# Optimization experiments

Hardware: AMD Instinct MI355X
Metric: run time of the kernel (lower is better)

Reference implementation:

```python
import jax, jax.numpy as jnp
import numpy as np

B, M, N_CTR, K = 16, 2048, 512, 32
DIM, DEPTH, HEADS = 384, 6, 6
EMB = 48  # fourier embedding dim (48//6 = 8 freqs per axis, basis [3,24])


def make_basis():
    e = (2.0 ** np.arange(EMB // 6)).astype(np.float32) * np.pi  # [8]
    z = np.zeros(EMB // 6, np.float32)
    basis = np.stack([np.concatenate([e, z, z]),
                      np.concatenate([z, e, z]),
                      np.concatenate([z, z, e])])  # [3, 24]
    return jnp.asarray(basis)


def fourier_embed(x, basis):
    # x [..., 3] -> [..., 48]  (sin/cos of 24 frequency projections)
    p = jnp.einsum('...d,de->...e', x, basis)
    return jnp.concatenate([jnp.sin(p), jnp.cos(p)], axis=-1)


def fps_idx(pos, n):
    # farthest point sampling, deterministic start at index 0. pos [M,3] -> [n]
    d0 = jnp.sum((pos - pos[0]) ** 2, -1)
    def step(d, _):
        i = jnp.argmax(d)
        d = jnp.minimum(d, jnp.sum((pos - pos[i]) ** 2, -1))
        return d, i
    _, idxs = jax.lax.scan(step, d0, None, length=n - 1)
    return jnp.concatenate([jnp.zeros(1, jnp.int32), idxs.astype(jnp.int32)])


def layernorm(x, g, b, eps=1e-6):
    m = jnp.mean(x, -1, keepdims=True)
    v = jnp.var(x, -1, keepdims=True)
    return (x - m) * jax.lax.rsqrt(v + eps) * g + b


def _lin(key, fi, fo):
    kw, kb = jax.random.split(key)
    w = jax.random.normal(kw, (fi, fo), jnp.float32) / np.sqrt(fi)
    b = jax.random.normal(kb, (fo,), jnp.float32) * 0.01
    return w, b


def setup_inputs() -> dict:
    key = jax.random.key(0)
    ks = jax.random.split(key, 16)
    pc = jax.random.uniform(ks[0], (B, M, 3), jnp.float32)
    embed_w, embed_b = _lin(ks[1], 3 + EMB, DIM)
    lw1, lb1 = _lin(ks[2], 3 + EMB, 256)
    lw2, lb2 = _lin(ks[3], 256, 256)
    gw1, gb1 = _lin(ks[4], 256, 256)
    gw2, gb2 = _lin(ks[5], 256, DIM)
    def stack_lin(k, fi, fo):
        kk = jax.random.split(k, DEPTH)
        ws, bs = zip(*[_lin(kk[i], fi, fo) for i in range(DEPTH)])
        return jnp.stack(ws), jnp.stack(bs)
    qkv_w, qkv_b = stack_lin(ks[6], DIM, 3 * DIM)
    proj_w, proj_b = stack_lin(ks[7], DIM, DIM)
    fc1_w, fc1_b = stack_lin(ks[8], DIM, 4 * DIM)
    fc2_w, fc2_b = stack_lin(ks[9], 4 * DIM, DIM)
    return dict(
        pc=pc, embed_w=embed_w, embed_b=embed_b,
        lw1=lw1, lb1=lb1, lw2=lw2, lb2=lb2,
        gw1=gw1, gb1=gb1, gw2=gw2, gb2=gb2,
        ln1_g=jnp.ones((DEPTH, DIM)), ln1_b=jnp.zeros((DEPTH, DIM)),
        qkv_w=qkv_w, qkv_b=qkv_b, proj_w=proj_w, proj_b=proj_b,
        gamma1=jax.random.normal(ks[10], (DEPTH, DIM)) * 0.1,
        ln2_g=jnp.ones((DEPTH, DIM)), ln2_b=jnp.zeros((DEPTH, DIM)),
        fc1_w=fc1_w, fc1_b=fc1_b, fc2_w=fc2_w, fc2_b=fc2_b,
        gamma2=jax.random.normal(ks[11], (DEPTH, DIM)) * 0.1,
        lnf_g=jnp.ones((DIM,)), lnf_b=jnp.zeros((DIM,)),
    )


def reference(pc, embed_w, embed_b, lw1, lb1, lw2, lb2, gw1, gb1, gw2, gb2,
              ln1_g, ln1_b, qkv_w, qkv_b, proj_w, proj_b, gamma1,
              ln2_g, ln2_b, fc1_w, fc1_b, fc2_w, fc2_b, gamma2, lnf_g, lnf_b):
    basis = make_basis()
    # --- FPS centers (per batch) ---
    idx = jax.vmap(lambda p: fps_idx(p, N_CTR))(pc)                 # [B,N]
    centers = jnp.take_along_axis(pc, idx[:, :, None], axis=1)      # [B,N,3]
    # --- KNN graph: for each center, K nearest of the M points ---
    d2 = jnp.sum((centers[:, :, None, :] - pc[:, None, :, :]) ** 2, -1)  # [B,N,M]
    _, nn_idx = jax.lax.top_k(-d2, K)                               # [B,N,K]
    # --- PointConv: gather -> local MLP -> max-scatter -> global MLP ---
    src = jax.vmap(lambda p, i: p[i])(pc, nn_idx)                   # [B,N,K,3]
    rel = src - centers[:, :, None, :]
    feat = jnp.concatenate([rel, fourier_embed(rel, basis)], -1)    # [B,N,K,51]
    h = jax.nn.relu(feat @ lw1 + lb1) @ lw2 + lb2                   # [B,N,K,256]
    h = jnp.max(h, axis=2)  # scatter_max over edges == max over K neighbors
    x = jax.nn.relu(h @ gw1 + gb1) @ gw2 + gb2                      # [B,N,DIM]
    # --- positional embedding tokens ---
    pe = jnp.concatenate([centers, fourier_embed(centers, basis)], -1) @ embed_w + embed_b
    x = x + pe
    # --- ViT blocks (pre-LN, LayerScale, eval mode: no dropout/droppath) ---
    hd = DIM // HEADS
    scale = hd ** -0.5
    for l in range(DEPTH):
        xn = layernorm(x, ln1_g[l], ln1_b[l])
        qkv = (xn @ qkv_w[l] + qkv_b[l]).reshape(B, N_CTR, 3, HEADS, hd)
        q, k, v = jnp.moveaxis(qkv, 2, 0)                           # [B,N,H,hd]
        att = jax.nn.softmax(jnp.einsum('bqhd,bkhd->bhqk', q, k) * scale, axis=-1)
        o = jnp.einsum('bhqk,bkhd->bqhd', att, v).reshape(B, N_CTR, DIM)
        x = x + gamma1[l] * (o @ proj_w[l] + proj_b[l])
        xn = layernorm(x, ln2_g[l], ln2_b[l])
        mlp = jax.nn.gelu(xn @ fc1_w[l] + fc1_b[l], approximate=False) @ fc2_w[l] + fc2_b[l]
        x = x + gamma2[l] * mlp
    out = layernorm(x, lnf_g, lnf_b)
    return out, centers
```

## Files before the change

### kernel.cpp

```cpp
#include <hip/hip_runtime.h>
#include <math.h>

#define NB 16
#define NM 2048
#define NCTR 512
#define NK 32
#define NDIM 384

typedef unsigned long long ull;
typedef unsigned int uint;
typedef unsigned short ushort;
typedef __attribute__((ext_vector_type(8))) short bf16x8;
typedef __attribute__((ext_vector_type(4))) float f32x4;

__device__ __forceinline__ float dist2_exact(float ax, float ay, float az,
                                             float bx, float by, float bz) {
  float dx = __fsub_rn(ax, bx);
  float dy = __fsub_rn(ay, by);
  float dz = __fsub_rn(az, bz);
  return __fadd_rn(__fadd_rn(__fmul_rn(dx, dx), __fmul_rn(dy, dy)),
                   __fmul_rn(dz, dz));
}

__device__ __forceinline__ float gelu_f(float x) {
  return 0.5f * x * (1.0f + erff(x * 0.70710678118654752f));
}

__device__ __forceinline__ ushort f2bf(float f) {
  uint u = __float_as_uint(f);
  return (ushort)((u + 0x7FFFu + ((u >> 16) & 1u)) >> 16);
}
__device__ __forceinline__ float bf2f(ushort h) {
  return __uint_as_float(((uint)h) << 16);
}

__device__ __forceinline__ void cvt8(float4 p, float4 q, uint4& hi, uint4& lo) {
  float v0 = p.x, v1 = p.y, v2 = p.z, v3 = p.w;
  float v4 = q.x, v5 = q.y, v6 = q.z, v7 = q.w;
  ushort h0 = f2bf(v0), h1 = f2bf(v1), h2 = f2bf(v2), h3 = f2bf(v3);
  ushort h4 = f2bf(v4), h5 = f2bf(v5), h6 = f2bf(v6), h7 = f2bf(v7);
  ushort l0 = f2bf(v0 - bf2f(h0)), l1 = f2bf(v1 - bf2f(h1));
  ushort l2 = f2bf(v2 - bf2f(h2)), l3 = f2bf(v3 - bf2f(h3));
  ushort l4 = f2bf(v4 - bf2f(h4)), l5 = f2bf(v5 - bf2f(h5));
  ushort l6 = f2bf(v6 - bf2f(h6)), l7 = f2bf(v7 - bf2f(h7));
  hi.x = (uint)h0 | ((uint)h1 << 16); hi.y = (uint)h2 | ((uint)h3 << 16);
  hi.z = (uint)h4 | ((uint)h5 << 16); hi.w = (uint)h6 | ((uint)h7 << 16);
  lo.x = (uint)l0 | ((uint)l1 << 16); lo.y = (uint)l2 | ((uint)l3 << 16);
  lo.z = (uint)l4 | ((uint)l5 << 16); lo.w = (uint)l6 | ((uint)l7 << 16);
}

__device__ __forceinline__ void split_store(float v, ushort* H, ushort* L,
                                            size_t off) {
  ushort hi = f2bf(v);
  H[off] = hi;
  L[off] = f2bf(v - bf2f(hi));
}

__device__ __forceinline__ void gload16(const ushort* g, ushort* l) {
  __builtin_amdgcn_global_load_lds(
      (const __attribute__((address_space(1))) void*)g,
      (__attribute__((address_space(3))) void*)l, 16, 0, 0);
}

__global__ __launch_bounds__(256)
void fps_kernel(const float* __restrict__ pc, float* __restrict__ centers) {
  int b = blockIdx.x;
  __shared__ float4 pos4[NM];
  __shared__ ull red[2][4];
  const float* pb = pc + (size_t)b * (NM * 3);
  int tid = threadIdx.x, lane = tid & 63, wv = tid >> 6;
  float px[8], py[8], pz[8];
#pragma unroll
  for (int i = 0; i < 8; ++i) {
    int p = tid + 256 * i;
    float x = pb[3 * p], y = pb[3 * p + 1], z = pb[3 * p + 2];
    px[i] = x; py[i] = y; pz[i] = z;
    pos4[p] = make_float4(x, y, z, 0.f);
  }
  __syncthreads();
  float* cb = centers + (size_t)b * (NCTR * 3);
  float4 s0 = pos4[0];
  float sx = s0.x, sy = s0.y, sz = s0.z;
  if (tid == 0) { cb[0] = sx; cb[1] = sy; cb[2] = sz; }
  float d[8];
  for (int n = 1; n < NCTR; ++n) {
    ull best = 0;
#pragma unroll
    for (int i = 0; i < 8; ++i) {
      int p = tid + 256 * i;
      float nd = dist2_exact(px[i], py[i], pz[i], sx, sy, sz);
      d[i] = (n == 1) ? nd : fminf(d[i], nd);
      ull key = ((ull)__float_as_uint(d[i]) << 32) | (unsigned)(0x7FFFFFFF - p);
      best = best > key ? best : key;
    }
    float dl = __uint_as_float((uint)(best >> 32));
    float wm = dl;
#pragma unroll
    for (int off = 32; off; off >>= 1) wm = fmaxf(wm, __shfl_xor(wm, off));
    ull mask = __ballot(dl == wm);
    ull wkey;
    if (mask & (mask - 1)) {
      wkey = best;
#pragma unroll
      for (int off = 32; off; off >>= 1) {
        ull o = __shfl_xor(wkey, off);
        wkey = wkey > o ? wkey : o;
      }
    } else {
      int src = __ffsll((long long)mask) - 1;
      wkey = __shfl(best, src);
    }
    if (lane == 0) red[n & 1][wv] = wkey;
    __syncthreads();
    ull g0 = red[n & 1][0], g1 = red[n & 1][1];
    ull g2 = red[n & 1][2], g3 = red[n & 1][3];
    ull ga = g0 > g1 ? g0 : g1;
    ull gc2 = g2 > g3 ? g2 : g3;
    ull gb = ga > gc2 ? ga : gc2;
    int j = 0x7FFFFFFF - (int)(unsigned)(gb & 0xFFFFFFFFull);
    float4 np = pos4[j];
    sx = np.x; sy = np.y; sz = np.z;
    if (tid == 0) { cb[n * 3] = sx; cb[n * 3 + 1] = sy; cb[n * 3 + 2] = sz; }
  }
}

__global__ __launch_bounds__(256, 2)
void knn_kernel(const float* __restrict__ pc, const float* __restrict__ centers,
                int* __restrict__ nn) {
  __shared__ float pos[NM * 3];
  int b = blockIdx.x >> 7;
  int n0 = (blockIdx.x & 127) << 2;
  const float* pb = pc + (size_t)b * (NM * 3);
  for (int i = threadIdx.x; i < NM * 3; i += 256) pos[i] = pb[i];
  __syncthreads();
  int wv = threadIdx.x >> 6, lane = threadIdx.x & 63;
  int gc = b * NCTR + n0 + wv;
  float cx = centers[gc * 3], cy = centers[gc * 3 + 1], cz = centers[gc * 3 + 2];
  ull key[32];
  ull gmin[4];
#pragma unroll
  for (int g = 0; g < 4; ++g) {
    gmin[g] = ~0ull;
#pragma unroll
    for (int i = 0; i < 8; ++i) {
      int r = g * 8 + i;
      int p = lane + (r << 6);
      float nd = dist2_exact(pos[3 * p], pos[3 * p + 1], pos[3 * p + 2], cx, cy, cz);
      key[r] = ((ull)__float_as_uint(nd) << 11) | (unsigned)p;
      gmin[g] = gmin[g] < key[r] ? gmin[g] : key[r];
    }
  }
  ull a01 = gmin[0] < gmin[1] ? gmin[0] : gmin[1];
  ull a23 = gmin[2] < gmin[3] ? gmin[2] : gmin[3];
  ull lmin = a01 < a23 ? a01 : a23;
  int* nnc = nn + (size_t)gc * NK;
  for (int round = 0; round < NK; ++round) {
    ull w = lmin;
#pragma unroll
    for (int off = 32; off; off >>= 1) {
      ull o = __shfl_xor(w, off);
      w = w < o ? w : o;
    }
    if (lmin == w) {
      nnc[round] = (int)(w & 2047ull);
#pragma unroll
      for (int g = 0; g < 4; ++g) {
        if (gmin[g] == w) {
          gmin[g] = ~0ull;
#pragma unroll
          for (int i = 0; i < 8; ++i) {
            int r = g * 8 + i;
            key[r] = (key[r] == w) ? ~0ull : key[r];
            gmin[g] = gmin[g] < key[r] ? gmin[g] : key[r];
          }
        }
      }
      ull b01 = gmin[0] < gmin[1] ? gmin[0] : gmin[1];
      ull b23 = gmin[2] < gmin[3] ? gmin[2] : gmin[3];
      lmin = b01 < b23 ? b01 : b23;
    }
  }
}

__global__ __launch_bounds__(256)
void wconv(const float* __restrict__ W, ushort* __restrict__ out, int K8, int N,
           int Ksrc) {
  int c = blockIdx.x * 256 + threadIdx.x;
  if (c >= K8 * N) return;
  int kb = c / N, n = c - kb * N;
  float v[8];
#pragma unroll
  for (int i = 0; i < 8; ++i) {
    int row = kb * 8 + i;
    v[i] = (row < Ksrc) ? W[(size_t)row * N + n] : 0.f;
  }
  float4 p, q;
  p.x = v[0]; p.y = v[1]; p.z = v[2]; p.w = v[3];
  q.x = v[4]; q.y = v[5]; q.z = v[6]; q.w = v[7];
  uint4 hi, lo;
  cvt8(p, q, hi, lo);
  *(uint4*)(out + (size_t)c * 8) = hi;
  *(uint4*)(out + (size_t)(K8 * N + c) * 8) = lo;
}

__global__ __launch_bounds__(256, 2)
void edge_mfma(const float* __restrict__ pc, const float* __restrict__ centers,
               const int* __restrict__ nn, const ushort* __restrict__ lw1s,
               const float* __restrict__ lb1, const ushort* __restrict__ lw2s,
               const float* __restrict__ lb2, ushort* __restrict__ hH,
               ushort* __restrict__ hL) {
  __shared__ __align__(16) ushort featH[4096], featL[4096];
  __shared__ __align__(16) ushort t1H[16384], t1L[16384];
  int tid = threadIdx.x;
  int w = tid >> 6, lane = tid & 63;
  int l15 = lane & 15, l4 = lane >> 4;
  int wbase = w << 6;
  {
    int e = tid >> 2, s = tid & 3;
    int ge = blockIdx.x * 64 + e;
    int c = ge >> 5;
    int b = c >> 9;
    int j = nn[ge];
    const float* sp = pc + ((size_t)b * NM + j) * 3;
    float rx = sp[0] - centers[c * 3];
    float ry = sp[1] - centers[c * 3 + 1];
    float rz = sp[2] - centers[c * 3 + 2];
    auto putk = [&](int k, float v) {
      ushort hi = f2bf(v);
      ushort lo = f2bf(v - bf2f(hi));
      int idx = ((k >> 3) * 64 + e) * 8 + (k & 7);
      featH[idx] = hi;
      featL[idx] = lo;
    };
    if (s < 3) {
      float r = (s == 0) ? rx : (s == 1) ? ry : rz;
#pragma unroll
      for (int f = 0; f < 8; ++f) {
        float ef = (float)(M_PI * (double)(1 << f));
        float p = r * ef;
        putk(3 + 8 * s + f, sinf(p));
        putk(27 + 8 * s + f, cosf(p));
      }
    } else {
      putk(0, rx);
      putk(1, ry);
      putk(2, rz);
#pragma unroll
      for (int k = 51; k < 64; ++k) putk(k, 0.f);
    }
  }
  __syncthreads();
  const ushort* lw1H = lw1s;
  const ushort* lw1L = lw1s + 8 * 256 * 8;
  f32x4 acc1[4][4];
#pragma unroll
  for (int i = 0; i < 4; ++i)
#pragma unroll
    for (int j = 0; j < 4; ++j) acc1[i][j] = (f32x4){0.f, 0.f, 0.f, 0.f};
#pragma unroll
  for (int ks = 0; ks < 2; ++ks) {
    bf16x8 ah[4], al[4];
#pragma unroll
    for (int fm = 0; fm < 4; ++fm) {
      int idx = ((ks * 4 + l4) * 64 + fm * 16 + l15) * 8;
      ah[fm] = *(const bf16x8*)&featH[idx];
      al[fm] = *(const bf16x8*)&featL[idx];
    }
#pragma unroll
    for (int fn = 0; fn < 4; ++fn) {
      int col = wbase + fn * 16 + l15;
      size_t boff = ((size_t)(ks * 4 + l4) * 256 + col) * 8;
      bf16x8 bh = *(const bf16x8*)(lw1H + boff);
      bf16x8 bl = *(const bf16x8*)(lw1L + boff);
#pragma unroll
      for (int fm = 0; fm < 4; ++fm) {
        acc1[fm][fn] = __builtin_amdgcn_mfma_f32_16x16x32_bf16(al[fm], bh, acc1[fm][fn], 0, 0, 0);
        acc1[fm][fn] = __builtin_amdgcn_mfma_f32_16x16x32_bf16(ah[fm], bl, acc1[fm][fn], 0, 0, 0);
        acc1[fm][fn] = __builtin_amdgcn_mfma_f32_16x16x32_bf16(ah[fm], bh, acc1[fm][fn], 0, 0, 0);
      }
    }
  }
#pragma unroll
  for (int fn = 0; fn < 4; ++fn) {
    int chan = wbase + fn * 16 + l15;
    float bias = lb1[chan];
    int kb = chan >> 3, k7 = chan & 7;
#pragma unroll
    for (int fm = 0; fm < 4; ++fm) {
#pragma unroll
      for (int r = 0; r < 4; ++r) {
        int edge = fm * 16 + l4 * 4 + r;
        float v = fmaxf(acc1[fm][fn][r] + bias, 0.f);
        ushort hi = f2bf(v);
        ushort lo = f2bf(v - bf2f(hi));
        int idx = (kb * 64 + edge) * 8 + k7;
        t1H[idx] = hi;
        t1L[idx] = lo;
      }
    }
  }
  __syncthreads();
  const ushort* lw2H = lw2s;
  const ushort* lw2L = lw2s + 32 * 256 * 8;
  f32x4 acc2[4][4];
#pragma unroll
  for (int i = 0; i < 4; ++i)
#pragma unroll
    for (int j = 0; j < 4; ++j) acc2[i][j] = (f32x4){0.f, 0.f, 0.f, 0.f};
#pragma unroll
  for (int ks = 0; ks < 8; ++ks) {
    bf16x8 ah[4], al[4];
#pragma unroll
    for (int fm = 0; fm < 4; ++fm) {
      int idx = ((ks * 4 + l4) * 64 + fm * 16 + l15) * 8;
      ah[fm] = *(const bf16x8*)&t1H[idx];
      al[fm] = *(const bf16x8*)&t1L[idx];
    }
#pragma unroll
    for (int fn = 0; fn < 4; ++fn) {
      int col = wbase + fn * 16 + l15;
      size_t boff = ((size_t)(ks * 4 + l4) * 256 + col) * 8;
      bf16x8 bh = *(const bf16x8*)(lw2H + boff);
      bf16x8 bl = *(const bf16x8*)(lw2L + boff);
#pragma unroll
      for (int fm = 0; fm < 4; ++fm) {
        acc2[fm][fn] = __builtin_amdgcn_mfma_f32_16x16x32_bf16(al[fm], bh, acc2[fm][fn], 0, 0, 0);
        acc2[fm][fn] = __builtin_amdgcn_mfma_f32_16x16x32_bf16(ah[fm], bl, acc2[fm][fn], 0, 0, 0);
        acc2[fm][fn] = __builtin_amdgcn_mfma_f32_16x16x32_bf16(ah[fm], bh, acc2[fm][fn], 0, 0, 0);
      }
    }
  }
#pragma unroll
  for (int fn = 0; fn < 4; ++fn) {
    int col = wbase + fn * 16 + l15;
    float m0 = -INFINITY, m1 = -INFINITY;
#pragma unroll
    for (int r = 0; r < 4; ++r) {
      m0 = fmaxf(m0, fmaxf(acc2[0][fn][r], acc2[1][fn][r]));
      m1 = fmaxf(m1, fmaxf(acc2[2][fn][r], acc2[3][fn][r]));
    }
    m0 = fmaxf(m0, __shfl_xor(m0, 16));
    m0 = fmaxf(m0, __shfl_xor(m0, 32));
    m1 = fmaxf(m1, __shfl_xor(m1, 16));
    m1 = fmaxf(m1, __shfl_xor(m1, 32));
    if (l4 == 0) {
      float bias = lb2[col];
      int c0 = blockIdx.x * 2;
      split_store(m0 + bias, hH, hL, (size_t)c0 * 256 + col);
      split_store(m1 + bias, hH, hL, (size_t)(c0 + 1) * 256 + col);
    }
  }
}

template <int EPI, int OUTS, int BM>
__global__ __launch_bounds__(256, 2)
void gemm_s(const ushort* __restrict__ AH, const ushort* __restrict__ AL,
            const ushort* __restrict__ Wh, const ushort* __restrict__ Wl,
            const float* __restrict__ bias, const float* __restrict__ gamma,
            const float* __restrict__ resid, float* __restrict__ C,
            ushort* __restrict__ CH, ushort* __restrict__ CL,
            int M, int N, int K) {
  constexpr int WC = (BM == 128) ? 2 : 4;
  constexpr int FN = 128 / (WC * 16);
  constexpr int ACH = BM / 64;
  __shared__ __align__(16) ushort Ah[BM * 32], Al[BM * 32];
  __shared__ __align__(16) ushort Bh[4096], Bl[4096];
  int tid = threadIdx.x;
  int bn = blockIdx.x << 7, bm = blockIdx.y * BM;
  int wid = tid >> 6, lane = tid & 63;
  int wr = (BM == 128) ? (wid >> 1) : 0;
  int wc = (BM == 128) ? (wid & 1) : wid;
  int l15 = lane & 15, l4 = lane >> 4;

  f32x4 acc[4][FN];
#pragma unroll
  for (int i = 0; i < 4; ++i)
#pragma unroll
    for (int j = 0; j < FN; ++j) acc[i][j] = (f32x4){0.f, 0.f, 0.f, 0.f};

  int nkt = K >> 5;
  for (int kt = 0; kt < nkt; ++kt) {
#pragma unroll
    for (int q = 0; q < ACH; ++q) {
      int e = q * 256 + tid;
      int kb = e / BM, row = e % BM;
      size_t so = (size_t)(bm + row) * K + kt * 32 + kb * 8;
      gload16(AH + so, &Ah[e * 8]);
      gload16(AL + so, &Al[e * 8]);
    }
#pragma unroll
    for (int q = 0; q < 2; ++q) {
      int e = q * 256 + tid;
      int kb = e >> 7, n = e & 127;
      size_t so = ((size_t)(kt * 4 + kb) * N + bn + n) * 8;
      gload16(Wh + so, &Bh[e * 8]);
      gload16(Wl + so, &Bl[e * 8]);
    }
    __syncthreads();
    bf16x8 ahf[4], alf[4];
#pragma unroll
    for (int fm = 0; fm < 4; ++fm) {
      int ci = l4 * BM + wr * 64 + fm * 16 + l15;
      ahf[fm] = *(bf16x8*)&Ah[ci * 8];
      alf[fm] = *(bf16x8*)&Al[ci * 8];
    }
#pragma unroll
    for (int fn = 0; fn < FN; ++fn) {
      int ci = l4 * 128 + wc * (FN * 16) + fn * 16 + l15;
      bf16x8 bh = *(bf16x8*)&Bh[ci * 8];
      bf16x8 bl = *(bf16x8*)&Bl[ci * 8];
#pragma unroll
      for (int fm = 0; fm < 4; ++fm) {
        acc[fm][fn] = __builtin_amdgcn_mfma_f32_16x16x32_bf16(alf[fm], bh, acc[fm][fn], 0, 0, 0);
        acc[fm][fn] = __builtin_amdgcn_mfma_f32_16x16x32_bf16(ahf[fm], bl, acc[fm][fn], 0, 0, 0);
        acc[fm][fn] = __builtin_amdgcn_mfma_f32_16x16x32_bf16(ahf[fm], bh, acc[fm][fn], 0, 0, 0);
      }
    }
    __syncthreads();
  }

#pragma unroll
  for (int fn = 0; fn < FN; ++fn) {
    int col = bn + wc * (FN * 16) + fn * 16 + l15;
    float bv = bias[col];
    float gv = (EPI == 3) ? gamma[col] : 0.f;
#pragma unroll
    for (int fm = 0; fm < 4; ++fm) {
      int row0 = bm + wr * 64 + fm * 16 + l4 * 4;
#pragma unroll
      for (int r = 0; r < 4; ++r) {
        float v = acc[fm][fn][r] + bv;
        if (EPI == 1) v = fmaxf(v, 0.f);
        else if (EPI == 2) v = gelu_f(v);
        else if (EPI == 3) v = resid[(size_t)(row0 + r) * N + col] + gv * v;
        size_t off = (size_t)(row0 + r) * N + col;
        if (OUTS == 0) C[off] = v;
        else split_store(v, CH, CL, off);
      }
    }
  }
}

__global__ __launch_bounds__(256)
void pe_add(const float* __restrict__ centers, const float* __restrict__ ew,
            const float* __restrict__ eb, float* x) {
  __shared__ float fc[51];
  int c = blockIdx.x, tid = threadIdx.x;
  if (tid < 24) {
    int a = tid >> 3, f = tid & 7;
    float coord = centers[c * 3 + a];
    float p = coord * (float)(M_PI * (double)(1 << f));
    fc[3 + tid] = sinf(p);
    fc[27 + tid] = cosf(p);
  } else if (tid < 27) {
    fc[tid - 24] = centers[c * 3 + (tid - 24)];
  }
  __syncthreads();
  for (int j = tid; j < NDIM; j += 256) {
    float acc = eb[j];
#pragma unroll
    for (int d = 0; d < 51; ++d) acc = fmaf(fc[d], ew[d * NDIM + j], acc);
    x[(size_t)c * NDIM + j] += acc;
  }
}

__global__ __launch_bounds__(256)
void ln_f32(const float* __restrict__ x, const float* __restrict__ g,
            const float* __restrict__ b, float* __restrict__ y) {
  int row = (blockIdx.x << 2) + (threadIdx.x >> 6);
  int lane = threadIdx.x & 63;
  const float* xr = x + (size_t)row * NDIM;
  float v[6];
#pragma unroll
  for (int i = 0; i < 6; ++i) v[i] = xr[lane + (i << 6)];
  float s = 0.f;
#pragma unroll
  for (int i = 0; i < 6; ++i) s += v[i];
#pragma unroll
  for (int off = 32; off; off >>= 1) s += __shfl_xor(s, off);
  float m = s / 384.f;
  float var = 0.f;
#pragma unroll
  for (int i = 0; i < 6; ++i) { float dd = v[i] - m; var += dd * dd; }
#pragma unroll
  for (int off = 32; off; off >>= 1) var += __shfl_xor(var, off);
  var = var / 384.f;
  float rs = 1.f / sqrtf(var + 1e-6f);
#pragma unroll
  for (int i = 0; i < 6; ++i) {
    int cc = lane + (i << 6);
    y[(size_t)row * NDIM + cc] = (v[i] - m) * rs * g[cc] + b[cc];
  }
}

__global__ __launch_bounds__(256)
void ln_split(const float* __restrict__ x, const float* __restrict__ g,
              const float* __restrict__ b, ushort* __restrict__ yH,
              ushort* __restrict__ yL) {
  int row = (blockIdx.x << 2) + (threadIdx.x >> 6);
  int lane = threadIdx.x & 63;
  const float* xr = x + (size_t)row * NDIM;
  float v[6];
#pragma unroll
  for (int i = 0; i < 6; ++i) v[i] = xr[lane + (i << 6)];
  float s = 0.f;
#pragma unroll
  for (int i = 0; i < 6; ++i) s += v[i];
#pragma unroll
  for (int off = 32; off; off >>= 1) s += __shfl_xor(s, off);
  float m = s / 384.f;
  float var = 0.f;
#pragma unroll
  for (int i = 0; i < 6; ++i) { float dd = v[i] - m; var += dd * dd; }
#pragma unroll
  for (int off = 32; off; off >>= 1) var += __shfl_xor(var, off);
  var = var / 384.f;
  float rs = 1.f / sqrtf(var + 1e-6f);
#pragma unroll
  for (int i = 0; i < 6; ++i) {
    int cc = lane + (i << 6);
    float yv = (v[i] - m) * rs * g[cc] + b[cc];
    split_store(yv, yH, yL, (size_t)row * NDIM + cc);
  }
}

__global__ __launch_bounds__(256, 2)
void attn_mfma(const ushort* __restrict__ FH, const ushort* __restrict__ FL,
               ushort* __restrict__ oH, ushort* __restrict__ oL) {
  __shared__ __align__(16) ushort kTH[4096], kTL[4096];
  __shared__ __align__(16) ushort vSH[4096], vSL[4096];
  __shared__ __align__(16) ushort pSH[8192], pSL[8192];
  int bi = blockIdx.x;
  int qt = bi & 3;
  int hh = (bi >> 2) % 6;
  int b = bi / 24;
  int tid = threadIdx.x;
  int w = tid >> 6, lane = tid & 63;
  int l15 = lane & 15, l4 = lane >> 4;
  const ushort* baseH = FH + (size_t)(b * NCTR) * 1152;
  const ushort* baseL = FL + (size_t)(b * NCTR) * 1152;
  int qbase = qt * 128 + w * 32;

  bf16x8 qh[2][2], ql[2][2];
#pragma unroll
  for (int qr = 0; qr < 2; ++qr) {
#pragma unroll
    for (int ds = 0; ds < 2; ++ds) {
      size_t off = (size_t)(qbase + qr * 16 + l15) * 1152 + hh * 64 + ds * 32 + l4 * 8;
      qh[qr][ds] = *(const bf16x8*)(baseH + off);
      ql[qr][ds] = *(const bf16x8*)(baseL + off);
    }
  }

  f32x4 oacc[2][4];
#pragma unroll
  for (int i = 0; i < 2; ++i)
#pragma unroll
    for (int j = 0; j < 4; ++j) oacc[i][j] = (f32x4){0.f, 0.f, 0.f, 0.f};
  float m_[2][4], l_[2][4];
#pragma unroll
  for (int i = 0; i < 2; ++i)
#pragma unroll
    for (int r = 0; r < 4; ++r) { m_[i][r] = -INFINITY; l_[i][r] = 0.f; }

  ushort* pHw = pSH + w * 2048;
  ushort* pLw = pSL + w * 2048;

  for (int ch = 0; ch < 8; ++ch) {
    {
      int key = tid & 63, dgh = tid >> 6;
      size_t krow = (size_t)(ch * 64 + key) * 1152 + 384 + hh * 64;
#pragma unroll
      for (int i = 0; i < 2; ++i) {
        int dg = dgh * 2 + i;
        *(uint4*)&kTH[(dg * 64 + key) * 8] = *(const uint4*)(baseH + krow + dg * 8);
        *(uint4*)&kTL[(dg * 64 + key) * 8] = *(const uint4*)(baseL + krow + dg * 8);
      }
      int d = tid & 63, kb2 = tid >> 6;
#pragma unroll
      for (int i = 0; i < 2; ++i) {
        int kb = kb2 + i * 4;
        ushort hv[8], lv[8];
#pragma unroll
        for (int j = 0; j < 8; ++j) {
          size_t off = (size_t)(ch * 64 + kb * 8 + j) * 1152 + 768 + hh * 64 + d;
          hv[j] = baseH[off];
          lv[j] = baseL[off];
        }
        uint4 H, L;
        H.x = (uint)hv[0] | ((uint)hv[1] << 16); H.y = (uint)hv[2] | ((uint)hv[3] << 16);
        H.z = (uint)hv[4] | ((uint)hv[5] << 16); H.w = (uint)hv[6] | ((uint)hv[7] << 16);
        L.x = (uint)lv[0] | ((uint)lv[1] << 16); L.y = (uint)lv[2] | ((uint)lv[3] << 16);
        L.z = (uint)lv[4] | ((uint)lv[5] << 16); L.w = (uint)lv[6] | ((uint)lv[7] << 16);
        *(uint4*)&vSH[(kb * 64 + d) * 8] = H;
        *(uint4*)&vSL[(kb * 64 + d) * 8] = L;
      }
    }
    __syncthreads();

    f32x4 sacc[2][4];
#pragma unroll
    for (int i = 0; i < 2; ++i)
#pragma unroll
      for (int j = 0; j < 4; ++j) sacc[i][j] = (f32x4){0.f, 0.f, 0.f, 0.f};
#pragma unroll
    for (int ds = 0; ds < 2; ++ds) {
#pragma unroll
      for (int kc = 0; kc < 4; ++kc) {
        int idx = ((ds * 4 + l4) * 64 + kc * 16 + l15) * 8;
        bf16x8 bh = *(const bf16x8*)&kTH[idx];
        bf16x8 bl = *(const bf16x8*)&kTL[idx];
#pragma unroll
        for (int qr = 0; qr < 2; ++qr) {
          sacc[qr][kc] = __builtin_amdgcn_mfma_f32_16x16x32_bf16(ql[qr][ds], bh, sacc[qr][kc], 0, 0, 0);
          sacc[qr][kc] = __builtin_amdgcn_mfma_f32_16x16x32_bf16(qh[qr][ds], bl, sacc[qr][kc], 0, 0, 0);
          sacc[qr][kc] = __builtin_amdgcn_mfma_f32_16x16x32_bf16(qh[qr][ds], bh, sacc[qr][kc], 0, 0, 0);
        }
      }
    }

    float t[2][4];
#pragma unroll
    for (int qr = 0; qr < 2; ++qr)
#pragma unroll
      for (int r = 0; r < 4; ++r) {
        float a0 = sacc[qr][0][r] * 0.125f; sacc[qr][0][r] = a0;
        float a1 = sacc[qr][1][r] * 0.125f; sacc[qr][1][r] = a1;
        float a2 = sacc[qr][2][r] * 0.125f; sacc[qr][2][r] = a2;
        float a3 = sacc[qr][3][r] * 0.125f; sacc[qr][3][r] = a3;
        t[qr][r] = fmaxf(fmaxf(a0, a1), fmaxf(a2, a3));
      }
#pragma unroll
    for (int off = 1; off < 16; off <<= 1)
#pragma unroll
      for (int qr = 0; qr < 2; ++qr)
#pragma unroll
        for (int r = 0; r < 4; ++r)
          t[qr][r] = fmaxf(t[qr][r], __shfl_xor(t[qr][r], off));
    float f_[2][4];
#pragma unroll
    for (int qr = 0; qr < 2; ++qr)
#pragma unroll
      for (int r = 0; r < 4; ++r) {
        float mn = fmaxf(m_[qr][r], t[qr][r]);
        f_[qr][r] = expf(m_[qr][r] - mn);
        m_[qr][r] = mn;
      }
#pragma unroll
    for (int qr = 0; qr < 2; ++qr)
#pragma unroll
      for (int dc = 0; dc < 4; ++dc)
#pragma unroll
        for (int r = 0; r < 4; ++r) oacc[qr][dc][r] *= f_[qr][r];
    float sm[2][4];
#pragma unroll
    for (int qr = 0; qr < 2; ++qr)
#pragma unroll
      for (int r = 0; r < 4; ++r) {
        float p0 = expf(sacc[qr][0][r] - m_[qr][r]); sacc[qr][0][r] = p0;
        float p1 = expf(sacc[qr][1][r] - m_[qr][r]); sacc[qr][1][r] = p1;
        float p2 = expf(sacc[qr][2][r] - m_[qr][r]); sacc[qr][2][r] = p2;
        float p3 = expf(sacc[qr][3][r] - m_[qr][r]); sacc[qr][3][r] = p3;
        sm[qr][r] = ((p0 + p1) + (p2 + p3));
      }
#pragma unroll
    for (int off = 1; off < 16; off <<= 1)
#pragma unroll
      for (int qr = 0; qr < 2; ++qr)
#pragma unroll
        for (int r = 0; r < 4; ++r)
          sm[qr][r] += __shfl_xor(sm[qr][r], off);
#pragma unroll
    for (int qr = 0; qr < 2; ++qr)
#pragma unroll
      for (int r = 0; r < 4; ++r) l_[qr][r] = l_[qr][r] * f_[qr][r] + sm[qr][r];

#pragma unroll
    for (int qr = 0; qr < 2; ++qr)
#pragma unroll
      for (int kc = 0; kc < 4; ++kc)
#pragma unroll
        for (int r = 0; r < 4; ++r) {
          float pv = sacc[qr][kc][r];
          ushort hi = f2bf(pv);
          ushort lo = f2bf(pv - bf2f(hi));
          int k = kc * 16 + l15;
          int qrow = qr * 16 + l4 * 4 + r;
          int idx = ((k >> 3) * 32 + qrow) * 8 + (k & 7);
          pHw[idx] = hi;
          pLw[idx] = lo;
        }

#pragma unroll
    for (int ks = 0; ks < 2; ++ks) {
      bf16x8 pah[2], pal[2];
#pragma unroll
      for (int qr = 0; qr < 2; ++qr) {
        int idx = ((ks * 4 + l4) * 32 + qr * 16 + l15) * 8;
        pah[qr] = *(const bf16x8*)&pHw[idx];
        pal[qr] = *(const bf16x8*)&pLw[idx];
      }
#pragma unroll
      for (int dc = 0; dc < 4; ++dc) {
        int idx = ((ks * 4 + l4) * 64 + dc * 16 + l15) * 8;
        bf16x8 vh = *(const bf16x8*)&vSH[idx];
        bf16x8 vl = *(const bf16x8*)&vSL[idx];
#pragma unroll
        for (int qr = 0; qr < 2; ++qr) {
          oacc[qr][dc] = __builtin_amdgcn_mfma_f32_16x16x32_bf16(pal[qr], vh, oacc[qr][dc], 0, 0, 0);
          oacc[qr][dc] = __builtin_amdgcn_mfma_f32_16x16x32_bf16(pah[qr], vl, oacc[qr][dc], 0, 0, 0);
          oacc[qr][dc] = __builtin_amdgcn_mfma_f32_16x16x32_bf16(pah[qr], vh, oacc[qr][dc], 0, 0, 0);
        }
      }
    }
    __syncthreads();
  }

  float il[2][4];
#pragma unroll
  for (int qr = 0; qr < 2; ++qr)
#pragma unroll
    for (int r = 0; r < 4; ++r) il[qr][r] = 1.f / l_[qr][r];
#pragma unroll
  for (int qr = 0; qr < 2; ++qr)
#pragma unroll
    for (int dc = 0; dc < 4; ++dc)
#pragma unroll
      for (int r = 0; r < 4; ++r) {
        int row = b * NCTR + qbase + qr * 16 + l4 * 4 + r;
        int col = hh * 64 + dc * 16 + l15;
        split_store(oacc[qr][dc][r] * il[qr][r], oH, oL, (size_t)row * NDIM + col);
      }
}

extern "C" void kernel_launch(void* const* d_in, const int* in_sizes, int n_in,
                              void* d_out, int out_size, void* d_ws, size_t ws_size,
                              hipStream_t stream) {
  const float* pc      = (const float*)d_in[0];
  const float* embed_w = (const float*)d_in[1];
  const float* embed_b = (const float*)d_in[2];
  const float* lw1     = (const float*)d_in[3];
  const float* lb1     = (const float*)d_in[4];
  const float* lw2     = (const float*)d_in[5];
  const float* lb2     = (const float*)d_in[6];
  const float* gw1     = (const float*)d_in[7];
  const float* gb1     = (const float*)d_in[8];
  const float* gw2     = (const float*)d_in[9];
  const float* gb2     = (const float*)d_in[10];
  const float* ln1_g   = (const float*)d_in[11];
  const float* ln1_b   = (const float*)d_in[12];
  const float* qkv_w   = (const float*)d_in[13];
  const float* qkv_b   = (const float*)d_in[14];
  const float* proj_w  = (const float*)d_in[15];
  const float* proj_b  = (const float*)d_in[16];
  const float* gamma1  = (const float*)d_in[17];
  const float* ln2_g   = (const float*)d_in[18];
  const float* ln2_b   = (const float*)d_in[19];
  const float* fc1_w   = (const float*)d_in[20];
  const float* fc1_b   = (const float*)d_in[21];
  const float* fc2_w   = (const float*)d_in[22];
  const float* fc2_b   = (const float*)d_in[23];
  const float* gamma2  = (const float*)d_in[24];
  const float* lnf_g   = (const float*)d_in[25];
  const float* lnf_b   = (const float*)d_in[26];

  float* out = (float*)d_out;
  float* centers = out + (size_t)NB * NCTR * NDIM;

  char* ws = (char*)d_ws;
  int*    nn  = (int*)(ws + 0);
  float*  x   = (float*)(ws + 1048576);
  ushort* xnH = (ushort*)(ws + 13631488);
  ushort* xnL = (ushort*)(ws + 19922944);
  ushort* FH  = (ushort*)(ws + 26214400);
  ushort* FL  = (ushort*)(ws + 51380224);
  ushort* hH  = (ushort*)(ws + 76546048);
  ushort* hL  = (ushort*)(ws + 80740352);
  ushort* wsplit = (ushort*)(ws + 84934656);

  size_t wofs = 0;
  auto convp = [&](const float* w, int Kpad, int N, int Ksrc) -> ushort* {
    ushort* dst = wsplit + wofs;
    int K8 = Kpad >> 3, total = K8 * N;
    wconv<<<(total + 255) / 256, 256, 0, stream>>>(w, dst, K8, N, Ksrc);
    wofs += (size_t)2 * Kpad * N;
    return dst;
  };
  ushort* qkvS = convp(qkv_w, 2304, 1152, 2304);
  ushort* projS = convp(proj_w, 2304, 384, 2304);
  ushort* fc1S = convp(fc1_w, 2304, 1536, 2304);
  ushort* fc2S = convp(fc2_w, 9216, 384, 9216);
  ushort* g1S  = convp(gw1, 256, 256, 256);
  ushort* g2S  = convp(gw2, 256, 384, 256);
  ushort* lw1s = convp(lw1, 64, 256, 51);
  ushort* lw2s = convp(lw2, 256, 256, 256);

  fps_kernel<<<NB, 256, 0, stream>>>(pc, centers);
  knn_kernel<<<2048, 256, 0, stream>>>(pc, centers, nn);
  edge_mfma<<<4096, 256, 0, stream>>>(pc, centers, nn, lw1s, lb1, lw2s, lb2, hH, hL);

  gemm_s<1, 1, 64><<<dim3(2, 128), 256, 0, stream>>>(
      hH, hL, g1S, g1S + 65536, gb1, nullptr, nullptr, nullptr, xnH, xnL,
      8192, 256, 256);
  gemm_s<0, 0, 64><<<dim3(3, 128), 256, 0, stream>>>(
      xnH, xnL, g2S, g2S + 98304, gb2, nullptr, nullptr, x, nullptr, nullptr,
      8192, 384, 256);
  pe_add<<<8192, 256, 0, stream>>>(centers, embed_w, embed_b, x);

  for (int l = 0; l < 6; ++l) {
    ln_split<<<2048, 256, 0, stream>>>(x, ln1_g + l * 384, ln1_b + l * 384, xnH, xnL);
    gemm_s<0, 1, 128><<<dim3(9, 64), 256, 0, stream>>>(
        xnH, xnL, qkvS + (size_t)l * 442368, qkvS + 2654208 + (size_t)l * 442368,
        qkv_b + l * 1152, nullptr, nullptr, nullptr, FH, FL, 8192, 1152, 384);
    attn_mfma<<<384, 256, 0, stream>>>(FH, FL, xnH, xnL);
    gemm_s<3, 0, 64><<<dim3(3, 128), 256, 0, stream>>>(
        xnH, xnL, projS + (size_t)l * 147456, projS + 884736 + (size_t)l * 147456,
        proj_b + l * 384, gamma1 + l * 384, x, x, nullptr, nullptr, 8192, 384, 384);
    ln_split<<<2048, 256, 0, stream>>>(x, ln2_g + l * 384, ln2_b + l * 384, xnH, xnL);
    gemm_s<2, 1, 128><<<dim3(12, 64), 256, 0, stream>>>(
        xnH, xnL, fc1S + (size_t)l * 589824, fc1S + 3538944 + (size_t)l * 589824,
        fc1_b + l * 1536, nullptr, nullptr, nullptr, FH, FL, 8192, 1536, 384);
    gemm_s<3, 0, 64><<<dim3(3, 128), 256, 0, stream>>>(
        FH, FL, fc2S + (size_t)l * 589824, fc2S + 3538944 + (size_t)l * 589824,
        fc2_b + l * 384, gamma2 + l * 384, x, x, nullptr, nullptr, 8192, 384, 1536);
  }
  ln_f32<<<2048, 256, 0, stream>>>(x, lnf_g, lnf_b, out);
}
```

Before: 2.145 ms.

## Double-buffer GEMM shared tiles and merge weight conversions into one launch

The split-bf16 GEMM now keeps two shared-memory buffers for the A and B tiles. It issues the loads for the next K tile right after the barrier, so global-to-LDS traffic overlaps the MFMA work on the current tile, and one barrier per iteration is removed. The eight separate weight-conversion launches are folded into a single kernel that looks up its source and destination from a block-offset table. Shared memory use per block doubles, which may lower occupancy below the launch bound of 2 blocks per CU.

```diff
diff --git a/kernel.cpp b/kernel.cpp
--- a/kernel.cpp
+++ b/kernel.cpp
@@ -182,11 +182,26 @@
   }
 }
 
+struct WAll {
+  const float* src[8];
+  ushort* dst[8];
+  int K8[8];
+  int N[8];
+  int Ksrc[8];
+  int blk0[9];
+};
+
 __global__ __launch_bounds__(256)
-void wconv(const float* __restrict__ W, ushort* __restrict__ out, int K8, int N,
-           int Ksrc) {
-  int c = blockIdx.x * 256 + threadIdx.x;
+void wconv8(WAll a) {
+  int bid = blockIdx.x;
+  int f = 0;
+#pragma unroll
+  for (int i = 1; i < 8; ++i) f += (bid >= a.blk0[i]);
+  int K8 = a.K8[f], N = a.N[f], Ksrc = a.Ksrc[f];
+  int c = (bid - a.blk0[f]) * 256 + threadIdx.x;
   if (c >= K8 * N) return;
+  const float* W = a.src[f];
+  ushort* out = a.dst[f];
   int kb = c / N, n = c - kb * N;
   float v[8];
 #pragma unroll
@@ -363,8 +378,8 @@
   constexpr int WC = (BM == 128) ? 2 : 4;
   constexpr int FN = 128 / (WC * 16);
   constexpr int ACH = BM / 64;
-  __shared__ __align__(16) ushort Ah[BM * 32], Al[BM * 32];
-  __shared__ __align__(16) ushort Bh[4096], Bl[4096];
+  __shared__ __align__(16) ushort Ah[2][BM * 32], Al[2][BM * 32];
+  __shared__ __align__(16) ushort Bh[2][4096], Bl[2][4096];
   int tid = threadIdx.x;
   int bn = blockIdx.x << 7, bm = blockIdx.y * BM;
   int wid = tid >> 6, lane = tid & 63;
@@ -378,37 +393,43 @@
 #pragma unroll
     for (int j = 0; j < FN; ++j) acc[i][j] = (f32x4){0.f, 0.f, 0.f, 0.f};
 
-  int nkt = K >> 5;
-  for (int kt = 0; kt < nkt; ++kt) {
+  auto stage = [&](int buf, int kt) {
 #pragma unroll
     for (int q = 0; q < ACH; ++q) {
       int e = q * 256 + tid;
       int kb = e / BM, row = e % BM;
       size_t so = (size_t)(bm + row) * K + kt * 32 + kb * 8;
-      gload16(AH + so, &Ah[e * 8]);
-      gload16(AL + so, &Al[e * 8]);
+      gload16(AH + so, &Ah[buf][e * 8]);
+      gload16(AL + so, &Al[buf][e * 8]);
     }
 #pragma unroll
     for (int q = 0; q < 2; ++q) {
       int e = q * 256 + tid;
       int kb = e >> 7, n = e & 127;
       size_t so = ((size_t)(kt * 4 + kb) * N + bn + n) * 8;
-      gload16(Wh + so, &Bh[e * 8]);
-      gload16(Wl + so, &Bl[e * 8]);
-    }
+      gload16(Wh + so, &Bh[buf][e * 8]);
+      gload16(Wl + so, &Bl[buf][e * 8]);
+    }
+  };
+
+  int nkt = K >> 5;
+  stage(0, 0);
+  for (int kt = 0; kt < nkt; ++kt) {
+    int cur = kt & 1;
     __syncthreads();
+    if (kt + 1 < nkt) stage(cur ^ 1, kt + 1);
     bf16x8 ahf[4], alf[4];
 #pragma unroll
     for (int fm = 0; fm < 4; ++fm) {
       int ci = l4 * BM + wr * 64 + fm * 16 + l15;
-      ahf[fm] = *(bf16x8*)&Ah[ci * 8];
-      alf[fm] = *(bf16x8*)&Al[ci * 8];
+      ahf[fm] = *(bf16x8*)&Ah[cur][ci * 8];
+      alf[fm] = *(bf16x8*)&Al[cur][ci * 8];
     }
 #pragma unroll
     for (int fn = 0; fn < FN; ++fn) {
       int ci = l4 * 128 + wc * (FN * 16) + fn * 16 + l15;
-      bf16x8 bh = *(bf16x8*)&Bh[ci * 8];
-      bf16x8 bl = *(bf16x8*)&Bl[ci * 8];
+      bf16x8 bh = *(bf16x8*)&Bh[cur][ci * 8];
+      bf16x8 bl = *(bf16x8*)&Bl[cur][ci * 8];
 #pragma unroll
       for (int fm = 0; fm < 4; ++fm) {
         acc[fm][fn] = __builtin_amdgcn_mfma_f32_16x16x32_bf16(alf[fm], bh, acc[fm][fn], 0, 0, 0);
@@ -416,7 +437,6 @@
         acc[fm][fn] = __builtin_amdgcn_mfma_f32_16x16x32_bf16(ahf[fm], bh, acc[fm][fn], 0, 0, 0);
       }
     }
-    __syncthreads();
   }
 
 #pragma unroll
@@ -778,22 +798,35 @@
   ushort* hL  = (ushort*)(ws + 80740352);
   ushort* wsplit = (ushort*)(ws + 84934656);
 
+  WAll wa;
+  const float* srcs[8] = {qkv_w, proj_w, fc1_w, fc2_w, gw1, gw2, lw1, lw2};
+  int kpads[8] = {2304, 2304, 2304, 9216, 256, 256, 64, 256};
+  int ns[8]    = {1152, 384, 1536, 384, 256, 384, 256, 256};
+  int ksrcs[8] = {2304, 2304, 2304, 9216, 256, 256, 51, 256};
+  ushort* dsts[8];
   size_t wofs = 0;
-  auto convp = [&](const float* w, int Kpad, int N, int Ksrc) -> ushort* {
-    ushort* dst = wsplit + wofs;
-    int K8 = Kpad >> 3, total = K8 * N;
-    wconv<<<(total + 255) / 256, 256, 0, stream>>>(w, dst, K8, N, Ksrc);
-    wofs += (size_t)2 * Kpad * N;
-    return dst;
-  };
-  ushort* qkvS = convp(qkv_w, 2304, 1152, 2304);
-  ushort* projS = convp(proj_w, 2304, 384, 2304);
-  ushort* fc1S = convp(fc1_w, 2304, 1536, 2304);
-  ushort* fc2S = convp(fc2_w, 9216, 384, 9216);
-  ushort* g1S  = convp(gw1, 256, 256, 256);
-  ushort* g2S  = convp(gw2, 256, 384, 256);
-  ushort* lw1s = convp(lw1, 64, 256, 51);
-  ushort* lw2s = convp(lw2, 256, 256, 256);
+  int cum = 0;
+  for (int f = 0; f < 8; ++f) {
+    dsts[f] = wsplit + wofs;
+    wofs += (size_t)2 * kpads[f] * ns[f];
+    wa.src[f] = srcs[f];
+    wa.dst[f] = dsts[f];
+    wa.K8[f] = kpads[f] >> 3;
+    wa.N[f] = ns[f];
+    wa.Ksrc[f] = ksrcs[f];
+    wa.blk0[f] = cum;
+    cum += ((kpads[f] >> 3) * ns[f] + 255) / 256;
+  }
+  wa.blk0[8] = cum;
+  wconv8<<<cum, 256, 0, stream>>>(wa);
+  ushort* qkvS = dsts[0];
+  ushort* projS = dsts[1];
+  ushort* fc1S = dsts[2];
+  ushort* fc2S = dsts[3];
+  ushort* g1S = dsts[4];
+  ushort* g2S = dsts[5];
+  ushort* lw1s = dsts[6];
+  ushort* lw2s = dsts[7];
 
   fps_kernel<<<NB, 256, 0, stream>>>(pc, centers);
   knn_kernel<<<2048, 256, 0, stream>>>(pc, centers, nn);
```

After: 2.213 ms. 3.2% more time.
